# Optimization experiments

Hardware: AMD Instinct MI355X
Metric: run time of the kernel (lower is better)

The kernel has to match this reference:

```python
import jax, jax.numpy as jnp
import numpy as np

B, M, D, H, F, N = 8, 1024, 1024, 16, 4096, 4
DK = D // H
EPS = 1e-5


def _ln(x, g, b):
    mu = jnp.mean(x, axis=-1, keepdims=True)
    var = jnp.mean(jnp.square(x - mu), axis=-1, keepdims=True)
    return (x - mu) * jax.lax.rsqrt(var + EPS) * g + b


def setup_inputs() -> dict:
    key = jax.random.key(0)
    ks = jax.random.split(key, 12)
    s = 0.02
    return {
        "embeds": jax.random.normal(ks[0], (B, M, D), dtype=jnp.float32),
        "weights": jax.random.normal(ks[1], (B, M), dtype=jnp.float32) * 0.1,
        "Wq": jax.random.normal(ks[2], (N, D, D), dtype=jnp.float32) * s,
        "bq": jnp.zeros((N, D), dtype=jnp.float32),
        "Wk": jax.random.normal(ks[3], (N, D, D), dtype=jnp.float32) * s,
        "bk": jnp.zeros((N, D), dtype=jnp.float32),
        "Wv": jax.random.normal(ks[4], (N, D, D), dtype=jnp.float32) * s,
        "bv": jnp.zeros((N, D), dtype=jnp.float32),
        "Wo": jax.random.normal(ks[5], (N, D, D), dtype=jnp.float32) * s,
        "bo": jnp.zeros((N, D), dtype=jnp.float32),
        "W1": jax.random.normal(ks[6], (N, D, F), dtype=jnp.float32) * s,
        "b1": jnp.zeros((N, F), dtype=jnp.float32),
        "W2": jax.random.normal(ks[7], (N, F, D), dtype=jnp.float32) * s,
        "b2": jnp.zeros((N, D), dtype=jnp.float32),
        "g1": jnp.ones((N, D), dtype=jnp.float32),
        "be1": jnp.zeros((N, D), dtype=jnp.float32),
        "g2": jnp.ones((N, D), dtype=jnp.float32),
        "be2": jnp.zeros((N, D), dtype=jnp.float32),
    }


def reference(embeds, weights, Wq, bq, Wk, bk, Wv, bv, Wo, bo,
              W1, b1, W2, b2, g1, be1, g2, be2):
    scale = 1.0 / np.sqrt(DK).astype(np.float32)
    bias = weights[:, None, None, :]  # b,1,1,m additive bias over keys

    def layer(x, p):
        wq, bq_, wk, bk_, wv, bv_, wo, bo_, w1, b1_, w2, b2_, g1_, be1_, g2_, be2_ = p
        q = (x @ wq + bq_).reshape(B, M, H, DK)
        k = (x @ wk + bk_).reshape(B, M, H, DK)
        v = (x @ wv + bv_).reshape(B, M, H, DK)
        scores = jnp.einsum("bqhd,bkhd->bhqk", q, k) * scale + bias
        attn = jax.nn.softmax(scores, axis=-1)
        o = jnp.einsum("bhqk,bkhd->bqhd", attn, v).reshape(B, M, D)
        o = o @ wo + bo_
        x = _ln(x + o, g1_, be1_)
        y = jax.nn.gelu(x @ w1 + b1_, approximate=False) @ w2 + b2_
        x = _ln(x + y, g2_, be2_)
        return x, None

    params = (Wq, bq, Wk, bk, Wv, bv, Wo, bo, W1, b1, W2, b2, g1, be1, g2, be2)
    out, _ = jax.lax.scan(layer, embeds, params)
    return out
```

## Files before the change

kernel.cpp:

```cpp
#include <hip/hip_runtime.h>
#include <hip/hip_bf16.h>

#define BB  8
#define MM  1024
#define DD  1024
#define HH  16
#define FF  4096
#define NL  4
#define DKK 64

typedef __bf16 bf16_t;
typedef __bf16 bf16x8 __attribute__((ext_vector_type(8)));
typedef __bf16 bf16x4 __attribute__((ext_vector_type(4)));
typedef float  f32x4  __attribute__((ext_vector_type(4)));

__device__ __forceinline__ void gld16(const bf16_t* g, bf16_t* l) {
    __builtin_amdgcn_global_load_lds((const __attribute__((address_space(1))) void*)g,
                                     (__attribute__((address_space(3))) void*)l,
                                     16, 0, 0);
}

__global__ __launch_bounds__(256) void cvt_x(const float* __restrict__ e,
                                             float* __restrict__ x,
                                             bf16_t* __restrict__ xb) {
    size_t i = ((size_t)blockIdx.x * 256 + threadIdx.x) * 4;
    float4 v = *(const float4*)(e + i);
    *(float4*)(x + i) = v;
    bf16x4 o;
    o[0] = (bf16_t)v.x; o[1] = (bf16_t)v.y; o[2] = (bf16_t)v.z; o[3] = (bf16_t)v.w;
    *(bf16x4*)(xb + i) = o;
}

__global__ __launch_bounds__(256) void transpose_all(const float* __restrict__ Wq,
                                                     const float* __restrict__ Wk,
                                                     const float* __restrict__ Wv,
                                                     const float* __restrict__ Wo,
                                                     const float* __restrict__ W1,
                                                     const float* __restrict__ W2,
                                                     bf16_t* __restrict__ qkvT,
                                                     bf16_t* __restrict__ WoT,
                                                     bf16_t* __restrict__ W1T,
                                                     bf16_t* __restrict__ W2T) {
    __shared__ float tile[32][33];
    const int bx = blockIdx.x;
    const float* in;
    bf16_t* out;
    int C, t;
    if (bx < 4096) {
        const int mat = bx >> 10;
        t = bx & 1023;
        C = 1024;
        in  = mat == 0 ? Wq : mat == 1 ? Wk : mat == 2 ? Wv : Wo;
        out = mat < 3 ? qkvT + (size_t)mat * DD * DD : WoT;
    } else if (bx < 8192) {
        t = bx - 4096; C = 4096; in = W1; out = W1T;
    } else {
        t = bx - 8192; C = 1024; in = W2; out = W2T;
    }
    const int cb = C >> 5;
    const int c0 = (t % cb) * 32, r0 = (t / cb) * 32;
    const int R = (C == 1024) ? ((bx < 8192) ? 1024 : 4096) : 1024;
    const int tx = threadIdx.x & 31, ty = threadIdx.x >> 5;
    for (int i = 0; i < 4; i++)
        tile[ty + i * 8][tx] = in[(size_t)(r0 + ty + i * 8) * C + c0 + tx];
    __syncthreads();
    for (int i = 0; i < 4; i++)
        out[(size_t)(c0 + ty + i * 8) * R + r0 + tx] = (bf16_t)tile[tx][ty + i * 8];
}

__global__ __launch_bounds__(256) void concat_bias(const float* __restrict__ bq,
                                                   const float* __restrict__ bk,
                                                   const float* __restrict__ bv,
                                                   float* __restrict__ out) {
    const int seg = blockIdx.x, l = blockIdx.y, t = threadIdx.x;
    const float* src = seg == 0 ? bq : seg == 1 ? bk : bv;
    float4 v = *(const float4*)(src + (size_t)l * 1024 + t * 4);
    *(float4*)(out + (size_t)l * 3072 + seg * 1024 + t * 4) = v;
}

__global__ __launch_bounds__(256) void transpose_v_k(const bf16_t* __restrict__ v,
                                                     bf16_t* __restrict__ vT, int ld) {
    __shared__ bf16_t t[64][65];
    int bh = blockIdx.y, b = bh >> 4, h = bh & 15;
    int m0 = blockIdx.x * 64;
    int tx = threadIdx.x & 63, ty = threadIdx.x >> 6;
    for (int i = 0; i < 16; i++) {
        int mr = ty * 16 + i;
        t[mr][tx] = v[(size_t)(b * MM + m0 + mr) * ld + h * DKK + tx];
    }
    __syncthreads();
    for (int i = 0; i < 16; i++) {
        int dk = ty * 16 + i;
        vT[((size_t)(bh * DKK + dk)) * MM + m0 + tx] = t[tx][dk];
    }
}

template <int EPI>
__global__ __launch_bounds__(256) void gemm_bt(const bf16_t* __restrict__ A,
                                               const bf16_t* __restrict__ Bt,
                                               const float* __restrict__ bias,
                                               const float* __restrict__ res,
                                               bf16_t* __restrict__ outb,
                                               float* __restrict__ outf,
                                               int K, int Ntot) {
    __shared__ bf16_t As[128 * 64];
    __shared__ bf16_t Bs[128 * 64];
    const int tid = threadIdx.x, wave = tid >> 6, lane = tid & 63;
    const int fr = lane & 15, quad = lane >> 4;
    const size_t bm = (size_t)blockIdx.y * 128, bn = (size_t)blockIdx.x * 128;
    const int wr = (wave >> 1) * 64, wc = (wave & 1) * 64;

    f32x4 acc[4][4] = {};

    const int sr8 = lane >> 3;
    const int sc8 = ((lane & 7) ^ sr8) * 8;
    const bf16_t* Ag = A + (bm + wave * 32 + sr8) * (size_t)K + sc8;
    const bf16_t* Bg = Bt + (bn + wave * 32 + sr8) * (size_t)K + sc8;
    bf16_t* Asw = &As[wave * 32 * 64];
    bf16_t* Bsw = &Bs[wave * 32 * 64];

    for (int k0 = 0; k0 < K; k0 += 64) {
        __syncthreads();
#pragma unroll
        for (int j = 0; j < 4; j++) {
            gld16(Ag + (size_t)(j * 8) * K + k0, Asw + j * 8 * 64);
            gld16(Bg + (size_t)(j * 8) * K + k0, Bsw + j * 8 * 64);
        }
        __syncthreads();
#pragma unroll
        for (int kk = 0; kk < 64; kk += 32) {
            bf16x8 af[4], bfr[4];
#pragma unroll
            for (int i = 0; i < 4; i++) {
                const int row = wr + i * 16 + fr;
                const int c8 = (kk >> 3) + quad;
                af[i] = *(const bf16x8*)&As[row * 64 + ((c8 ^ (row & 7)) << 3)];
            }
#pragma unroll
            for (int i = 0; i < 4; i++) {
                const int row = wc + i * 16 + fr;
                const int c8 = (kk >> 3) + quad;
                bfr[i] = *(const bf16x8*)&Bs[row * 64 + ((c8 ^ (row & 7)) << 3)];
            }
#pragma unroll
            for (int mi = 0; mi < 4; mi++)
#pragma unroll
                for (int ni = 0; ni < 4; ni++)
                    acc[mi][ni] = __builtin_amdgcn_mfma_f32_16x16x32_bf16(
                        af[mi], bfr[ni], acc[mi][ni], 0, 0, 0);
        }
    }

#pragma unroll
    for (int ni = 0; ni < 4; ni++) {
        const size_t c = bn + wc + ni * 16 + fr;
        const float bv = bias[c];
#pragma unroll
        for (int mi = 0; mi < 4; mi++) {
            const size_t rbase = bm + wr + mi * 16 + quad * 4;
#pragma unroll
            for (int r = 0; r < 4; r++) {
                const size_t idx = (rbase + r) * (size_t)Ntot + c;
                float v = acc[mi][ni][r] + bv;
                if constexpr (EPI == 0) {
                    outb[idx] = (bf16_t)v;
                } else if constexpr (EPI == 1) {
                    outf[idx] = v + res[idx];
                } else {
                    float g = 0.5f * v * (1.0f + erff(v * 0.70710678118654752f));
                    outb[idx] = (bf16_t)g;
                }
            }
        }
    }
}

__global__ __launch_bounds__(256) void flash_attn(const bf16_t* __restrict__ q,
                                                  const bf16_t* __restrict__ kmat,
                                                  const bf16_t* __restrict__ vT,
                                                  const float* __restrict__ wts,
                                                  bf16_t* __restrict__ ao, int ldq) {
    __shared__ bf16_t Ks[128 * 72];
    __shared__ bf16_t Vs[64 * 136];
    bf16_t* Ps = Ks;

    const int tid = threadIdx.x;
    const int wave = tid >> 6, lane = tid & 63;
    const int fr = lane & 15, quad = lane >> 4;
    const int fk = quad * 8;
    const int bh = blockIdx.y, b = bh >> 4, h = bh & 15;
    const int q0 = blockIdx.x * 64;

    const size_t qrow = (size_t)(b * MM + q0 + wave * 16 + fr) * ldq + h * DKK;
    const bf16x8 aq0 = *(const bf16x8*)(q + qrow + fk);
    const bf16x8 aq1 = *(const bf16x8*)(q + qrow + 32 + fk);

    f32x4 oacc[4] = {};
    float lrow[4] = {0.f, 0.f, 0.f, 0.f};

    for (int kt = 0; kt < MM; kt += 128) {
        __syncthreads();
#pragma unroll
        for (int rr = 0; rr < 4; rr++) {
            const int key = rr * 32 + (tid >> 3);
            const int dkc = (tid & 7) * 8;
            *(bf16x8*)(&Ks[key * 72 + dkc]) =
                *(const bf16x8*)(kmat + (size_t)(b * MM + kt + key) * ldq + h * DKK + dkc);
            const int dkr = rr * 16 + (tid >> 4);
            const int kc = (tid & 15) * 8;
            *(bf16x8*)(&Vs[dkr * 136 + kc]) =
                *(const bf16x8*)(vT + (size_t)(bh * DKK + dkr) * MM + kt + kc);
        }
        __syncthreads();

        f32x4 s[8];
#pragma unroll
        for (int ni = 0; ni < 8; ni++) {
            const bf16_t* kp = &Ks[(ni * 16 + fr) * 72];
            f32x4 z = {0.f, 0.f, 0.f, 0.f};
            z = __builtin_amdgcn_mfma_f32_16x16x32_bf16(aq0, *(const bf16x8*)(kp + fk), z, 0, 0, 0);
            z = __builtin_amdgcn_mfma_f32_16x16x32_bf16(aq1, *(const bf16x8*)(kp + 32 + fk), z, 0, 0, 0);
            const float wv = wts[b * MM + kt + ni * 16 + fr];
#pragma unroll
            for (int r = 0; r < 4; r++) s[ni][r] = __expf(z[r] * 0.125f + wv);
        }

        float rs[4] = {0.f, 0.f, 0.f, 0.f};
#pragma unroll
        for (int ni = 0; ni < 8; ni++)
#pragma unroll
            for (int r = 0; r < 4; r++) rs[r] += s[ni][r];
#pragma unroll
        for (int off = 1; off < 16; off <<= 1)
#pragma unroll
            for (int r = 0; r < 4; r++) rs[r] += __shfl_xor(rs[r], off, 16);
#pragma unroll
        for (int r = 0; r < 4; r++) lrow[r] += rs[r];

        __syncthreads();

#pragma unroll
        for (int ni = 0; ni < 8; ni++)
#pragma unroll
            for (int r = 0; r < 4; r++)
                Ps[(wave * 16 + quad * 4 + r) * 136 + ni * 16 + fr] = (bf16_t)s[ni][r];

#pragma unroll
        for (int c2 = 0; c2 < 4; c2++) {
            const bf16x8 ap = *(const bf16x8*)(&Ps[(wave * 16 + fr) * 136 + c2 * 32 + fk]);
#pragma unroll
            for (int ni = 0; ni < 4; ni++) {
                const bf16x8 bv = *(const bf16x8*)(&Vs[(ni * 16 + fr) * 136 + c2 * 32 + fk]);
                oacc[ni] = __builtin_amdgcn_mfma_f32_16x16x32_bf16(ap, bv, oacc[ni], 0, 0, 0);
            }
        }
    }

    const size_t orow = (size_t)(b * MM + q0 + wave * 16 + quad * 4);
#pragma unroll
    for (int ni = 0; ni < 4; ni++)
#pragma unroll
        for (int r = 0; r < 4; r++) {
            const float ov = oacc[ni][r] / lrow[r];
            ao[(orow + r) * DD + h * DKK + ni * 16 + fr] = (bf16_t)ov;
        }
}

__global__ __launch_bounds__(256) void ln_k(const float* __restrict__ in,
                                            const float* __restrict__ g,
                                            const float* __restrict__ be,
                                            float* __restrict__ xout,
                                            bf16_t* __restrict__ xb) {
    const int row = blockIdx.x, t = threadIdx.x;
    const float* rp = in + (size_t)row * DD;
    float4 v = *(const float4*)(rp + t * 4);
    float s = v.x + v.y + v.z + v.w;
    float ss = v.x * v.x + v.y * v.y + v.z * v.z + v.w * v.w;
    for (int off = 1; off < 64; off <<= 1) {
        s += __shfl_xor(s, off);
        ss += __shfl_xor(ss, off);
    }
    __shared__ float sb[4], ssb[4];
    if ((t & 63) == 0) { sb[t >> 6] = s; ssb[t >> 6] = ss; }
    __syncthreads();
    s = sb[0] + sb[1] + sb[2] + sb[3];
    ss = ssb[0] + ssb[1] + ssb[2] + ssb[3];
    const float mu = s * (1.0f / DD);
    const float var = ss * (1.0f / DD) - mu * mu;
    const float rstd = rsqrtf(var + 1e-5f);
    float4 gg = *(const float4*)(g + t * 4);
    float4 bb = *(const float4*)(be + t * 4);
    float o0 = (v.x - mu) * rstd * gg.x + bb.x;
    float o1 = (v.y - mu) * rstd * gg.y + bb.y;
    float o2 = (v.z - mu) * rstd * gg.z + bb.z;
    float o3 = (v.w - mu) * rstd * gg.w + bb.w;
    *(float4*)(xout + (size_t)row * DD + t * 4) = make_float4(o0, o1, o2, o3);
    bf16x4 ob;
    ob[0] = (bf16_t)o0; ob[1] = (bf16_t)o1; ob[2] = (bf16_t)o2; ob[3] = (bf16_t)o3;
    *(bf16x4*)(xb + (size_t)row * DD + t * 4) = ob;
}

extern "C" void kernel_launch(void* const* d_in, const int* in_sizes, int n_in,
                              void* d_out, int out_size, void* d_ws, size_t ws_size,
                              hipStream_t stream) {
    const float* embeds = (const float*)d_in[0];
    const float* wts    = (const float*)d_in[1];
    const float* Wq = (const float*)d_in[2];
    const float* bq = (const float*)d_in[3];
    const float* Wk = (const float*)d_in[4];
    const float* bk = (const float*)d_in[5];
    const float* Wv = (const float*)d_in[6];
    const float* bv = (const float*)d_in[7];
    const float* Wo = (const float*)d_in[8];
    const float* bo = (const float*)d_in[9];
    const float* W1 = (const float*)d_in[10];
    const float* b1 = (const float*)d_in[11];
    const float* W2 = (const float*)d_in[12];
    const float* b2 = (const float*)d_in[13];
    const float* g1 = (const float*)d_in[14];
    const float* be1 = (const float*)d_in[15];
    const float* g2 = (const float*)d_in[16];
    const float* be2 = (const float*)d_in[17];
    float* x = (float*)d_out;

    char* p = (char*)d_ws;
    auto take = [&](size_t n) { char* r = p; p += (n + 255) & ~(size_t)255; return r; };
    const size_t nBMD = (size_t)BB * MM * DD;
    bf16_t* xb   = (bf16_t*)take(nBMD * 2);
    bf16_t* qkvb = (bf16_t*)take(nBMD * 3 * 2);
    bf16_t* vTb  = (bf16_t*)take(nBMD * 2);
    float*  r1   = (float*)take(nBMD * 4);
    float*  x1   = (float*)take(nBMD * 4);
    bf16_t* hb   = (bf16_t*)take((size_t)BB * MM * FF * 2);
    bf16_t* qkvT = (bf16_t*)take((size_t)3 * DD * DD * 2);
    bf16_t* WoT  = (bf16_t*)take((size_t)DD * DD * 2);
    bf16_t* W1T  = (bf16_t*)take((size_t)DD * FF * 2);
    bf16_t* W2T  = (bf16_t*)take((size_t)DD * FF * 2);
    float*  qkvB = (float*)take((size_t)NL * 3072 * 4);
    bf16_t* aob  = hb;
    bf16_t* x1b  = xb;

    cvt_x<<<8192, 256, 0, stream>>>(embeds, x, xb);
    concat_bias<<<dim3(3, NL), 256, 0, stream>>>(bq, bk, bv, qkvB);

    const dim3 gemmQKV(3072 / 128, (BB * MM) / 128);
    const dim3 gemmDD(DD / 128, (BB * MM) / 128);
    const dim3 gemmF1(FF / 128, (BB * MM) / 128);

    for (int l = 0; l < NL; l++) {
        transpose_all<<<12288, 256, 0, stream>>>(
            Wq + (size_t)l * DD * DD, Wk + (size_t)l * DD * DD,
            Wv + (size_t)l * DD * DD, Wo + (size_t)l * DD * DD,
            W1 + (size_t)l * DD * FF, W2 + (size_t)l * FF * DD,
            qkvT, WoT, W1T, W2T);

        gemm_bt<0><<<gemmQKV, 256, 0, stream>>>(xb, qkvT, qkvB + (size_t)l * 3072,
                                                nullptr, qkvb, nullptr, DD, 3072);

        transpose_v_k<<<dim3(16, 128), 256, 0, stream>>>(qkvb + 2048, vTb, 3072);
        flash_attn<<<dim3(16, 128), 256, 0, stream>>>(qkvb, qkvb + 1024, vTb, wts, aob, 3072);

        gemm_bt<1><<<gemmDD, 256, 0, stream>>>(aob, WoT, bo + (size_t)l * DD, x, nullptr, r1, DD, DD);
        ln_k<<<BB * MM, 256, 0, stream>>>(r1, g1 + (size_t)l * DD, be1 + (size_t)l * DD, x1, x1b);

        gemm_bt<2><<<gemmF1, 256, 0, stream>>>(x1b, W1T, b1 + (size_t)l * FF, nullptr, hb, nullptr, DD, FF);
        gemm_bt<1><<<gemmDD, 256, 0, stream>>>(hb, W2T, b2 + (size_t)l * DD, x1, nullptr, r1, FF, DD);
        ln_k<<<BB * MM, 256, 0, stream>>>(r1, g2 + (size_t)l * DD, be2 + (size_t)l * DD, x, xb);
    }
}
```

Measured before the change: 2.118 ms.

## Replace 128x128 GEMM with 256x256 multi-stage pipelined kernel with XCD-aware block remap

Swaps the 128x128, 256-thread GEMM for a 256x256 tile kernel with 512 threads. It uses a four-stage LDS ring of 32-wide K planes, so global-to-LDS loads for later planes are issued while MFMAs run on the current one. Blocks are remapped so neighbouring tiles land on the same XCD, and MFMA issue priority is raised. The goal is more reuse per loaded byte and latency hiding, at the cost of far fewer blocks for the D x D GEMMs (128 blocks) and heavier register and LDS use.

```diff
diff --git a/kernel.cpp b/kernel.cpp
--- a/kernel.cpp
+++ b/kernel.cpp
@@ -95,73 +95,98 @@
     }
 }
 
+__device__ __forceinline__ void stage_plane(const bf16_t* __restrict__ G, int K,
+                                            size_t rbase, size_t kcol0,
+                                            bf16_t* lds, int w, int srow, int scol) {
+#pragma unroll
+    for (int j = 0; j < 2; j++)
+        gld16(G + (rbase + (size_t)(j * 128 + w * 16 + srow)) * (size_t)K + kcol0 + scol,
+              lds + j * 4096 + w * 512);
+}
+
 template <int EPI>
-__global__ __launch_bounds__(256) void gemm_bt(const bf16_t* __restrict__ A,
-                                               const bf16_t* __restrict__ Bt,
-                                               const float* __restrict__ bias,
-                                               const float* __restrict__ res,
-                                               bf16_t* __restrict__ outb,
-                                               float* __restrict__ outf,
-                                               int K, int Ntot) {
-    __shared__ bf16_t As[128 * 64];
-    __shared__ bf16_t Bs[128 * 64];
-    const int tid = threadIdx.x, wave = tid >> 6, lane = tid & 63;
+__global__ __launch_bounds__(512, 2) void gemm256(const bf16_t* __restrict__ A,
+                                                  const bf16_t* __restrict__ Bt,
+                                                  const float* __restrict__ bias,
+                                                  const float* __restrict__ res,
+                                                  bf16_t* __restrict__ outb,
+                                                  float* __restrict__ outf,
+                                                  int K, int Ntot) {
+    __shared__ __align__(16) bf16_t As[2 * 2 * 256 * 32];
+    __shared__ __align__(16) bf16_t Bs[2 * 2 * 256 * 32];
+    const int tid = threadIdx.x, w = tid >> 6, lane = tid & 63;
     const int fr = lane & 15, quad = lane >> 4;
-    const size_t bm = (size_t)blockIdx.y * 128, bn = (size_t)blockIdx.x * 128;
-    const int wr = (wave >> 1) * 64, wc = (wave & 1) * 64;
-
-    f32x4 acc[4][4] = {};
-
-    const int sr8 = lane >> 3;
-    const int sc8 = ((lane & 7) ^ sr8) * 8;
-    const bf16_t* Ag = A + (bm + wave * 32 + sr8) * (size_t)K + sc8;
-    const bf16_t* Bg = Bt + (bn + wave * 32 + sr8) * (size_t)K + sc8;
-    bf16_t* Asw = &As[wave * 32 * 64];
-    bf16_t* Bsw = &Bs[wave * 32 * 64];
-
-    for (int k0 = 0; k0 < K; k0 += 64) {
-        __syncthreads();
-#pragma unroll
-        for (int j = 0; j < 4; j++) {
-            gld16(Ag + (size_t)(j * 8) * K + k0, Asw + j * 8 * 64);
-            gld16(Bg + (size_t)(j * 8) * K + k0, Bsw + j * 8 * 64);
-        }
-        __syncthreads();
-#pragma unroll
-        for (int kk = 0; kk < 64; kk += 32) {
-            bf16x8 af[4], bfr[4];
-#pragma unroll
-            for (int i = 0; i < 4; i++) {
-                const int row = wr + i * 16 + fr;
-                const int c8 = (kk >> 3) + quad;
-                af[i] = *(const bf16x8*)&As[row * 64 + ((c8 ^ (row & 7)) << 3)];
-            }
-#pragma unroll
-            for (int i = 0; i < 4; i++) {
-                const int row = wc + i * 16 + fr;
-                const int c8 = (kk >> 3) + quad;
-                bfr[i] = *(const bf16x8*)&Bs[row * 64 + ((c8 ^ (row & 7)) << 3)];
-            }
-#pragma unroll
-            for (int mi = 0; mi < 4; mi++)
-#pragma unroll
-                for (int ni = 0; ni < 4; ni++)
-                    acc[mi][ni] = __builtin_amdgcn_mfma_f32_16x16x32_bf16(
-                        af[mi], bfr[ni], acc[mi][ni], 0, 0, 0);
-        }
-    }
-
-#pragma unroll
-    for (int ni = 0; ni < 4; ni++) {
-        const size_t c = bn + wc + ni * 16 + fr;
+    const int wm = w >> 2, wn = w & 3;
+    const int srow = lane >> 2;
+    const int scol = ((lane & 3) ^ ((lane >> 3) & 3)) << 3;
+    const int swz  = (quad ^ ((fr >> 1) & 3)) << 3;
+
+    const int gx = gridDim.x;
+    int lid = blockIdx.y * gx + blockIdx.x;
+    {
+        const int nwg = gx * gridDim.y;
+        const int qq = nwg >> 3, rr = nwg & 7, xc = lid & 7, lq = lid >> 3;
+        lid = (xc < rr ? xc * (qq + 1) : rr * (qq + 1) + (xc - rr) * qq) + lq;
+    }
+    const size_t bm = (size_t)(lid / gx) * 256;
+    const size_t bn = (size_t)(lid % gx) * 256;
+
+    const int NT = K >> 6;
+    f32x4 acc[8][4] = {};
+
+    stage_plane(A,  K, bm, 0,  As,         w, srow, scol);
+    stage_plane(Bt, K, bn, 0,  Bs,         w, srow, scol);
+    stage_plane(A,  K, bm, 32, As + 8192,  w, srow, scol);
+    stage_plane(Bt, K, bn, 32, Bs + 8192,  w, srow, scol);
+    stage_plane(A,  K, bm, 64, As + 16384, w, srow, scol);
+    stage_plane(Bt, K, bn, 64, Bs + 16384, w, srow, scol);
+    asm volatile("s_waitcnt vmcnt(8)\n\ts_barrier" ::: "memory");
+
+    auto phase = [&](int rdbase, int stbase, size_t stk) {
+        bf16x8 af[8], bfv[4];
+        const bf16_t* Ap = As + rdbase;
+        const bf16_t* Bp = Bs + rdbase;
+#pragma unroll
+        for (int i = 0; i < 8; i++)
+            af[i] = *(const bf16x8*)&Ap[(wm * 128 + i * 16 + fr) * 32 + swz];
+#pragma unroll
+        for (int j = 0; j < 4; j++)
+            bfv[j] = *(const bf16x8*)&Bp[(wn * 64 + j * 16 + fr) * 32 + swz];
+        stage_plane(A,  K, bm, stk, As + stbase, w, srow, scol);
+        stage_plane(Bt, K, bn, stk, Bs + stbase, w, srow, scol);
+        asm volatile("s_barrier" ::: "memory");
+        __builtin_amdgcn_s_setprio(1);
+#pragma unroll
+        for (int i = 0; i < 8; i++)
+#pragma unroll
+            for (int j = 0; j < 4; j++)
+                acc[i][j] = __builtin_amdgcn_mfma_f32_16x16x32_bf16(af[i], bfv[j],
+                                                                    acc[i][j], 0, 0, 0);
+        __builtin_amdgcn_s_setprio(0);
+        asm volatile("s_waitcnt vmcnt(8)\n\ts_barrier" ::: "memory");
+    };
+
+    for (int t = 0; t < NT; t += 2) {
+        const size_t t1 = (t + 1 < NT) ? t + 1 : NT - 1;
+        const size_t t2 = (t + 2 < NT) ? t + 2 : NT - 1;
+        const size_t t3 = (t + 3 < NT) ? t + 3 : NT - 1;
+        phase(0,     24576, t1 * 64 + 32);
+        phase(8192,  0,     t2 * 64);
+        phase(16384, 8192,  t2 * 64 + 32);
+        phase(24576, 16384, t3 * 64);
+    }
+
+#pragma unroll
+    for (int j = 0; j < 4; j++) {
+        const size_t c = bn + wn * 64 + j * 16 + fr;
         const float bv = bias[c];
 #pragma unroll
-        for (int mi = 0; mi < 4; mi++) {
-            const size_t rbase = bm + wr + mi * 16 + quad * 4;
+        for (int i = 0; i < 8; i++) {
+            const size_t rbase = bm + wm * 128 + i * 16 + quad * 4;
 #pragma unroll
             for (int r = 0; r < 4; r++) {
                 const size_t idx = (rbase + r) * (size_t)Ntot + c;
-                float v = acc[mi][ni][r] + bv;
+                float v = acc[i][j][r] + bv;
                 if constexpr (EPI == 0) {
                     outb[idx] = (bf16_t)v;
                 } else if constexpr (EPI == 1) {
@@ -343,9 +368,9 @@
     cvt_x<<<8192, 256, 0, stream>>>(embeds, x, xb);
     concat_bias<<<dim3(3, NL), 256, 0, stream>>>(bq, bk, bv, qkvB);
 
-    const dim3 gemmQKV(3072 / 128, (BB * MM) / 128);
-    const dim3 gemmDD(DD / 128, (BB * MM) / 128);
-    const dim3 gemmF1(FF / 128, (BB * MM) / 128);
+    const dim3 gQKV(3072 / 256, (BB * MM) / 256);
+    const dim3 gDD(DD / 256, (BB * MM) / 256);
+    const dim3 gF1(FF / 256, (BB * MM) / 256);
 
     for (int l = 0; l < NL; l++) {
         transpose_all<<<12288, 256, 0, stream>>>(
@@ -354,17 +379,17 @@
             W1 + (size_t)l * DD * FF, W2 + (size_t)l * FF * DD,
             qkvT, WoT, W1T, W2T);
 
-        gemm_bt<0><<<gemmQKV, 256, 0, stream>>>(xb, qkvT, qkvB + (size_t)l * 3072,
-                                                nullptr, qkvb, nullptr, DD, 3072);
+        gemm256<0><<<gQKV, 512, 0, stream>>>(xb, qkvT, qkvB + (size_t)l * 3072,
+                                             nullptr, qkvb, nullptr, DD, 3072);
 
         transpose_v_k<<<dim3(16, 128), 256, 0, stream>>>(qkvb + 2048, vTb, 3072);
         flash_attn<<<dim3(16, 128), 256, 0, stream>>>(qkvb, qkvb + 1024, vTb, wts, aob, 3072);
 
-        gemm_bt<1><<<gemmDD, 256, 0, stream>>>(aob, WoT, bo + (size_t)l * DD, x, nullptr, r1, DD, DD);
+        gemm256<1><<<gDD, 512, 0, stream>>>(aob, WoT, bo + (size_t)l * DD, x, nullptr, r1, DD, DD);
         ln_k<<<BB * MM, 256, 0, stream>>>(r1, g1 + (size_t)l * DD, be1 + (size_t)l * DD, x1, x1b);
 
-        gemm_bt<2><<<gemmF1, 256, 0, stream>>>(x1b, W1T, b1 + (size_t)l * FF, nullptr, hb, nullptr, DD, FF);
-        gemm_bt<1><<<gemmDD, 256, 0, stream>>>(hb, W2T, b2 + (size_t)l * DD, x1, nullptr, r1, FF, DD);
+        gemm256<2><<<gF1, 512, 0, stream>>>(x1b, W1T, b1 + (size_t)l * FF, nullptr, hb, nullptr, DD, FF);
+        gemm256<1><<<gDD, 512, 0, stream>>>(hb, W2T, b2 + (size_t)l * DD, x1, nullptr, r1, FF, DD);
         ln_k<<<BB * MM, 256, 0, stream>>>(r1, g2 + (size_t)l * DD, be2 + (size_t)l * DD, x, xb);
     }
 }
```

New measurement: 2.319 ms. 1.1x slower.
